# Performance work log

Measured on AMD Instinct MI355X. Metric: run time of the kernel, lower is better.

## Reference

```python
import jax, jax.numpy as jnp
import numpy as np

N = 150000
E = 600000
IN_DIM = 128
HID = 64


def setup_inputs() -> dict:
    key = jax.random.key(0)
    ks = jax.random.split(key, 8)
    obs = jax.random.normal(ks[0], (N, IN_DIM), dtype=jnp.float32)
    edge_index = jax.random.randint(ks[1], (2, E), 0, N, dtype=jnp.int64)
    # GCNConv / Linear parameters (PyTorch layout: W is [out, in])
    W1 = jax.random.normal(ks[2], (HID, IN_DIM), dtype=jnp.float32) / np.sqrt(IN_DIM)
    b1 = jnp.zeros((HID,), dtype=jnp.float32)
    W2 = jax.random.normal(ks[3], (HID, HID), dtype=jnp.float32) / np.sqrt(HID)
    b2 = jnp.zeros((HID,), dtype=jnp.float32)
    W3 = jax.random.normal(ks[4], (1, HID), dtype=jnp.float32) / np.sqrt(HID)
    b3 = jnp.zeros((1,), dtype=jnp.float32)
    return {"obs": obs, "edge_index": edge_index, "W1": W1, "b1": b1,
            "W2": W2, "b2": b2, "W3": W3, "b3": b3}


def _gcn_norm(edge_index, n):
    # PyG gcn_norm: add self-loops, symmetric normalization D^-1/2 A D^-1/2
    loops = jnp.arange(n, dtype=edge_index.dtype)
    row = jnp.concatenate([edge_index[0], loops])  # source
    col = jnp.concatenate([edge_index[1], loops])  # target
    deg = jax.ops.segment_sum(jnp.ones(row.shape[0], jnp.float32), col, num_segments=n)
    dinv = jnp.where(deg > 0, jax.lax.rsqrt(deg), 0.0)
    norm = dinv[row] * dinv[col]  # [E+N]
    return row, col, norm


def _gcn_conv(x, row, col, norm, n, W, b):
    # x' = lin(x); out[col] += norm * x'[row]; out += bias
    xw = x @ W.T                     # [N, out]
    msg = xw[row] * norm[:, None]    # gather + scale, [E+N, out]
    out = jax.ops.segment_sum(msg, col, num_segments=n)
    return out + b


def reference(obs, edge_index, W1, b1, W2, b2, W3, b3):
    n = obs.shape[0]
    row, col, norm = _gcn_norm(edge_index, n)
    h1 = jax.nn.relu(_gcn_conv(obs, row, col, norm, n, W1, b1))
    h2 = jax.nn.relu(_gcn_conv(h1, row, col, norm, n, W2, b2))
    out = h2 @ W3.T + b3             # [N, 1]
    out = out.reshape(-1, 15)[:, 3:].reshape(-1)  # drop first 3 of every 15
    return out
```

## Files before the change

kernel.cpp:

```cpp
#include <hip/hip_runtime.h>

#define NN 150000
#define NE 600000
#define IND 128
#define HID 64
#define KMAX 32
#define BSHIFT 8
#define NBUCK 586
#define SUBCAP 224
#define PARTB 293
#define GEMM_GRID ((NN + 63) / 64)
#define NOUT 120000

typedef short s16x8 __attribute__((ext_vector_type(8)));
typedef float f32x4 __attribute__((ext_vector_type(4)));

__device__ __forceinline__ unsigned f2bf(float f) {
    unsigned u = __float_as_uint(f);
    return (u + 0x7FFFu + ((u >> 16) & 1u)) >> 16;
}

#define ACC4(v, dr) \
    a0 = fmaf(__uint_as_float((v).x << 16), dr, a0); \
    a1 = fmaf(__uint_as_float((v).x & 0xFFFF0000u), dr, a1); \
    a2 = fmaf(__uint_as_float((v).y << 16), dr, a2); \
    a3 = fmaf(__uint_as_float((v).y & 0xFFFF0000u), dr, a3);

__global__ void k_zero(int* __restrict__ gcnt) {
    int t = blockIdx.x * 256 + threadIdx.x;
    if (t < NBUCK * 8) gcnt[t] = 0;
}

__global__ __launch_bounds__(256) void k_part(
        const int* __restrict__ rowv, const int* __restrict__ colv,
        int* __restrict__ gcnt, int2* __restrict__ ebuf) {
    __shared__ int hist[NBUCK];
    __shared__ int bases[NBUCK];
    int tid = threadIdx.x;
    for (int i = tid; i < NBUCK; i += 256) hist[i] = 0;
    __syncthreads();
    int4 r4[2], c4[2];
    int bk[8], sl[8];
    bool val[2];
    #pragma unroll
    for (int h = 0; h < 2; ++h) {
        int t = blockIdx.x * 512 + h * 256 + tid;
        val[h] = (t < NE / 4);
        if (val[h]) {
            r4[h] = ((const int4*)rowv)[t];
            c4[h] = ((const int4*)colv)[t];
            bk[4*h+0] = c4[h].x >> BSHIFT; sl[4*h+0] = atomicAdd(&hist[bk[4*h+0]], 1);
            bk[4*h+1] = c4[h].y >> BSHIFT; sl[4*h+1] = atomicAdd(&hist[bk[4*h+1]], 1);
            bk[4*h+2] = c4[h].z >> BSHIFT; sl[4*h+2] = atomicAdd(&hist[bk[4*h+2]], 1);
            bk[4*h+3] = c4[h].w >> BSHIFT; sl[4*h+3] = atomicAdd(&hist[bk[4*h+3]], 1);
        }
    }
    __syncthreads();
    int xcd = blockIdx.x & 7;
    for (int i = tid; i < NBUCK; i += 256)
        bases[i] = hist[i] ? atomicAdd(&gcnt[i * 8 + xcd], hist[i]) : 0;
    __syncthreads();
    #pragma unroll
    for (int h = 0; h < 2; ++h) {
        if (val[h]) {
            #pragma unroll
            for (int e = 0; e < 4; ++e) {
                int c = (e == 0) ? c4[h].x : (e == 1) ? c4[h].y : (e == 2) ? c4[h].z : c4[h].w;
                int r = (e == 0) ? r4[h].x : (e == 1) ? r4[h].y : (e == 2) ? r4[h].z : r4[h].w;
                int p = bases[bk[4*h+e]] + sl[4*h+e];
                if (p < SUBCAP) ebuf[(bk[4*h+e] * 8 + xcd) * SUBCAP + p] = make_int2(c, r);
            }
        }
    }
}

__global__ __launch_bounds__(256) void k_sort_gemm1(
        const float* __restrict__ obs, const float* __restrict__ W1,
        unsigned short* __restrict__ xs,
        const int* __restrict__ gcnt, const int2* __restrict__ ebuf,
        int* __restrict__ cursor, float* __restrict__ dinvf,
        int* __restrict__ csr_src) {
    __shared__ char smem[2 * 64 * IND * 2];
    int tid = threadIdx.x;
    if (blockIdx.x < NBUCK) {
        int k = blockIdx.x;
        int lo = k << BSHIFT;
        int* cnt = (int*)smem;
        cnt[tid] = 0;
        int lens[8];
        #pragma unroll
        for (int x = 0; x < 8; ++x) {
            int l = gcnt[k * 8 + x];
            lens[x] = l > SUBCAP ? SUBCAP : l;
        }
        __syncthreads();
        for (int x = 0; x < 8; ++x) {
            const int2* run = ebuf + (size_t)(k * 8 + x) * SUBCAP;
            for (int i = tid; i < lens[x]; i += 256) {
                int2 e = run[i];
                int s = atomicAdd(&cnt[e.x - lo], 1);
                if (s < KMAX) csr_src[e.x * KMAX + s] = e.y;
            }
        }
        __syncthreads();
        int n = lo + tid;
        if (n < NN) {
            cursor[n] = cnt[tid];
            dinvf[n] = rsqrtf((float)(cnt[tid] + 1));
        }
        return;
    }
    char* sA = smem;
    char* sW = smem + 64 * IND * 2;
    int base = (blockIdx.x - NBUCK) * 64;

    {
        const float4* Wsrc = (const float4*)W1;
        for (int idx = tid; idx < 64 * 32; idx += 256) {
            int row = idx >> 5, c4i = idx & 31;
            float4 w = Wsrc[idx];
            uint2 p;
            p.x = f2bf(w.x) | (f2bf(w.y) << 16);
            p.y = f2bf(w.z) | (f2bf(w.w) << 16);
            int byte = row * (IND * 2) + c4i * 8;
            byte ^= (row & 7) << 4;
            *(uint2*)(sW + byte) = p;
        }
    }
    {
        const float4* Xsrc = (const float4*)obs;
        for (int idx = tid; idx < 64 * 32; idx += 256) {
            int row = idx >> 5, c4i = idx & 31;
            int n = base + row; if (n >= NN) n = NN - 1;
            float4 v = Xsrc[(size_t)n * 32 + c4i];
            uint2 p;
            p.x = f2bf(v.x) | (f2bf(v.y) << 16);
            p.y = f2bf(v.z) | (f2bf(v.w) << 16);
            int byte = row * (IND * 2) + c4i * 8;
            byte ^= (row & 7) << 4;
            *(uint2*)(sA + byte) = p;
        }
    }
    __syncthreads();

    int wave = tid >> 6, lane = tid & 63;
    int wr = wave >> 1, wc = wave & 1;
    int r16 = lane & 15, kg = lane >> 4;

    f32x4 acc[2][2];
    #pragma unroll
    for (int i = 0; i < 2; ++i)
        #pragma unroll
        for (int j = 0; j < 2; ++j)
            acc[i][j] = (f32x4){0.f, 0.f, 0.f, 0.f};

    #pragma unroll
    for (int s = 0; s < IND / 32; ++s) {
        int kb = (s * 32 + kg * 8) * 2;
        s16x8 a[2], b[2];
        #pragma unroll
        for (int i = 0; i < 2; ++i) {
            int row = 32 * wr + 16 * i + r16;
            int byte = row * (IND * 2) + kb;
            byte ^= (row & 7) << 4;
            a[i] = *(const s16x8*)(sA + byte);
        }
        #pragma unroll
        for (int j = 0; j < 2; ++j) {
            int row = 32 * wc + 16 * j + r16;
            int byte = row * (IND * 2) + kb;
            byte ^= (row & 7) << 4;
            b[j] = *(const s16x8*)(sW + byte);
        }
        #pragma unroll
        for (int i = 0; i < 2; ++i)
            #pragma unroll
            for (int j = 0; j < 2; ++j)
                acc[i][j] = __builtin_amdgcn_mfma_f32_16x16x32_bf16(a[i], b[j], acc[i][j], 0, 0, 0);
    }

    __syncthreads();
    unsigned short* sC = (unsigned short*)sA;
    #pragma unroll
    for (int i = 0; i < 2; ++i) {
        #pragma unroll
        for (int r = 0; r < 4; ++r) {
            int nloc = 32 * wr + 16 * i + kg * 4 + r;
            #pragma unroll
            for (int j = 0; j < 2; ++j) {
                int c = 32 * wc + 16 * j + r16;
                sC[nloc * 64 + c] = (unsigned short)f2bf(acc[i][j][r]);
            }
        }
    }
    __syncthreads();
    {
        uint4* dst = (uint4*)(xs + (size_t)base * HID);
        const uint4* s4p = (const uint4*)sC;
        #pragma unroll
        for (int k2 = 0; k2 < 2; ++k2) {
            int idx = k2 * 256 + tid;
            if (base + (idx >> 3) < NN) dst[idx] = s4p[idx];
        }
    }
}

__global__ __launch_bounds__(256) void k_agg_gemm(
        const unsigned short* __restrict__ xs, const int* __restrict__ cursor,
        const float* __restrict__ dinvf, const int* __restrict__ csr_src,
        const float* __restrict__ bias, const float* __restrict__ W2,
        unsigned short* __restrict__ xs2) {
    __shared__ char smem[2 * 64 * HID * 2];
    char* sA = smem;
    char* sB = smem + 64 * HID * 2;
    int tid = threadIdx.x;
    int base = blockIdx.x * 64;

    {
        const float4* Wsrc = (const float4*)W2;
        for (int idx = tid; idx < 64 * 16; idx += 256) {
            int row = idx >> 4, c4i = idx & 15;
            float4 w = Wsrc[idx];
            uint2 p;
            p.x = f2bf(w.x) | (f2bf(w.y) << 16);
            p.y = f2bf(w.z) | (f2bf(w.w) << 16);
            int byte = row * (HID * 2) + c4i * 8;
            byte ^= (row & 7) << 4;
            *(uint2*)(sB + byte) = p;
        }
    }

    int lane = tid & 63;
    int l16 = lane & 15, gbase = lane & 48;
    int grp = tid >> 4;
    const uint2* src = (const uint2*)xs;
    float4 bb = ((const float4*)bias)[l16];

    int degA[4], cntA[4], idxA[4];
    uint2 svA[4];
    float drA[4];
    #pragma unroll
    for (int s4 = 0; s4 < 4; ++s4) {
        int node = base + s4 * 16 + grp;
        bool ok = node < NN;
        int nc = ok ? node : NN - 1;
        int deg = cursor[nc];
        degA[s4] = deg;
        cntA[s4] = ok ? (deg < KMAX ? deg : KMAX) : 0;
        idxA[s4] = csr_src[nc * KMAX + l16];
        svA[s4]  = src[(size_t)nc * 16 + l16];
    }
    #pragma unroll
    for (int s4 = 0; s4 < 4; ++s4) {
        drA[s4] = (l16 < cntA[s4]) ? dinvf[idxA[s4]] : 0.0f;
    }

    #pragma unroll
    for (int s4 = 0; s4 < 4; ++s4) {
        int row = s4 * 16 + grp;
        int node = base + row;
        int cnt = cntA[s4];
        float dn = rsqrtf((float)(degA[s4] + 1));
        uint2 sv = svA[s4];
        float a0 = __uint_as_float(sv.x << 16) * dn;
        float a1 = __uint_as_float(sv.x & 0xFFFF0000u) * dn;
        float a2 = __uint_as_float(sv.y << 16) * dn;
        float a3 = __uint_as_float(sv.y & 0xFFFF0000u) * dn;
        uint2 v[8];
        #pragma unroll
        for (int j = 0; j < 8; ++j) {
            int r = __shfl(idxA[s4], gbase + j, 64);
            r = (j < cnt) ? r : 0;
            v[j] = src[(size_t)r * 16 + l16];
        }
        #pragma unroll
        for (int j = 0; j < 8; ++j) {
            float dr = __shfl(drA[s4], gbase + j, 64);
            ACC4(v[j], dr)
        }
        if (cnt > 8) {
            int c16 = cnt < 16 ? cnt : 16;
            for (int j = 8; j < c16; ++j) {
                int r    = __shfl(idxA[s4], gbase + j, 64);
                float dr = __shfl(drA[s4], gbase + j, 64);
                uint2 vv = src[(size_t)r * 16 + l16];
                ACC4(vv, dr)
            }
            for (int j = 16; j < cnt; ++j) {
                int r = csr_src[node * KMAX + j];
                float dr = dinvf[r];
                uint2 vv = src[(size_t)r * 16 + l16];
                ACC4(vv, dr)
            }
        }
        float h0 = fmaxf(fmaf(dn, a0, bb.x), 0.f);
        float h1 = fmaxf(fmaf(dn, a1, bb.y), 0.f);
        float h2 = fmaxf(fmaf(dn, a2, bb.z), 0.f);
        float h3 = fmaxf(fmaf(dn, a3, bb.w), 0.f);
        uint2 o;
        o.x = f2bf(h0) | (f2bf(h1) << 16);
        o.y = f2bf(h2) | (f2bf(h3) << 16);
        if (node >= NN) { o.x = 0u; o.y = 0u; }
        int byte = row * (HID * 2) + l16 * 8;
        byte ^= (row & 7) << 4;
        *(uint2*)(sA + byte) = o;
    }
    __syncthreads();

    int wave = tid >> 6;
    int wr = wave >> 1, wc = wave & 1;
    int r16 = lane & 15, kg = lane >> 4;

    f32x4 acc[2][2];
    #pragma unroll
    for (int i = 0; i < 2; ++i)
        #pragma unroll
        for (int j = 0; j < 2; ++j)
            acc[i][j] = (f32x4){0.f, 0.f, 0.f, 0.f};

    #pragma unroll
    for (int s = 0; s < HID / 32; ++s) {
        int kb = (s * 32 + kg * 8) * 2;
        s16x8 a[2], bfr[2];
        #pragma unroll
        for (int i = 0; i < 2; ++i) {
            int row = 32 * wr + 16 * i + r16;
            int byte = row * (HID * 2) + kb;
            byte ^= (row & 7) << 4;
            a[i] = *(const s16x8*)(sA + byte);
        }
        #pragma unroll
        for (int j = 0; j < 2; ++j) {
            int row = 32 * wc + 16 * j + r16;
            int byte = row * (HID * 2) + kb;
            byte ^= (row & 7) << 4;
            bfr[j] = *(const s16x8*)(sB + byte);
        }
        #pragma unroll
        for (int i = 0; i < 2; ++i)
            #pragma unroll
            for (int j = 0; j < 2; ++j)
                acc[i][j] = __builtin_amdgcn_mfma_f32_16x16x32_bf16(a[i], bfr[j], acc[i][j], 0, 0, 0);
    }

    __syncthreads();
    unsigned short* sC = (unsigned short*)sA;
    #pragma unroll
    for (int i = 0; i < 2; ++i) {
        #pragma unroll
        for (int r = 0; r < 4; ++r) {
            int nloc = 32 * wr + 16 * i + kg * 4 + r;
            int n = base + nloc;
            float d = dinvf[n < NN ? n : NN - 1];
            #pragma unroll
            for (int j = 0; j < 2; ++j) {
                int c = 32 * wc + 16 * j + r16;
                sC[nloc * 64 + c] = (unsigned short)f2bf(acc[i][j][r] * d);
            }
        }
    }
    __syncthreads();
    {
        uint4* dst = (uint4*)(xs2 + (size_t)base * HID);
        const uint4* s4p = (const uint4*)sC;
        #pragma unroll
        for (int k2 = 0; k2 < 2; ++k2) {
            int idx = k2 * 256 + tid;
            if (base + (idx >> 3) < NN) dst[idx] = s4p[idx];
        }
    }
}

__global__ __launch_bounds__(256) void k_agg_out(const unsigned short* __restrict__ xs,
                      const int* __restrict__ cursor, const int* __restrict__ csr_src,
                      const float* __restrict__ bias, const float* __restrict__ W3,
                      const float* __restrict__ b3, float* __restrict__ outp) {
    int tid = threadIdx.x;
    int lane = tid & 63;
    int l16 = lane & 15, gbase = lane & 48;
    int q = blockIdx.x * 16 + (tid >> 4);
    if (q >= NOUT) return;
    int g15 = q / 12, jj12 = q - g15 * 12;
    int node = g15 * 15 + 3 + jj12;
    int deg = cursor[node];
    int cnt = deg < KMAX ? deg : KMAX;
    float dn = rsqrtf((float)(deg + 1));
    const uint2* src = (const uint2*)xs;
    int idx0 = csr_src[node * KMAX + l16];
    float w0 = (l16 < cnt) ? 1.0f : 0.0f;
    uint2 sv = src[(size_t)node * 16 + l16];
    float a0 = __uint_as_float(sv.x << 16);
    float a1 = __uint_as_float(sv.x & 0xFFFF0000u);
    float a2 = __uint_as_float(sv.y << 16);
    float a3 = __uint_as_float(sv.y & 0xFFFF0000u);
    uint2 v[8];
    #pragma unroll
    for (int j = 0; j < 8; ++j) {
        int r = __shfl(idx0, gbase + j, 64);
        r = (j < cnt) ? r : 0;
        v[j] = src[(size_t)r * 16 + l16];
    }
    #pragma unroll
    for (int j = 0; j < 8; ++j) {
        float w = __shfl(w0, gbase + j, 64);
        ACC4(v[j], w)
    }
    if (cnt > 8) {
        int c16 = cnt < 16 ? cnt : 16;
        for (int j = 8; j < c16; ++j) {
            int r = __shfl(idx0, gbase + j, 64);
            uint2 vv = src[(size_t)r * 16 + l16];
            ACC4(vv, 1.0f)
        }
        for (int j = 16; j < cnt; ++j) {
            int r = csr_src[node * KMAX + j];
            uint2 vv = src[(size_t)r * 16 + l16];
            ACC4(vv, 1.0f)
        }
    }
    float4 bb = ((const float4*)bias)[l16];
    float h0 = fmaxf(fmaf(dn, a0, bb.x), 0.f);
    float h1 = fmaxf(fmaf(dn, a1, bb.y), 0.f);
    float h2 = fmaxf(fmaf(dn, a2, bb.z), 0.f);
    float h3 = fmaxf(fmaf(dn, a3, bb.w), 0.f);
    float4 ww = ((const float4*)W3)[l16];
    float v3 = h0 * ww.x + h1 * ww.y + h2 * ww.z + h3 * ww.w;
    v3 += __shfl_xor(v3, 1, 64);
    v3 += __shfl_xor(v3, 2, 64);
    v3 += __shfl_xor(v3, 4, 64);
    v3 += __shfl_xor(v3, 8, 64);
    if (l16 == 0) outp[q] = v3 + b3[0];
}

extern "C" void kernel_launch(void* const* d_in, const int* in_sizes, int n_in,
                              void* d_out, int out_size, void* d_ws, size_t ws_size,
                              hipStream_t stream) {
    const float* obs = (const float*)d_in[0];
    const int*   ei  = (const int*)d_in[1];
    const float* W1  = (const float*)d_in[2];
    const float* b1  = (const float*)d_in[3];
    const float* W2  = (const float*)d_in[4];
    const float* b2  = (const float*)d_in[5];
    const float* W3  = (const float*)d_in[6];
    const float* b3  = (const float*)d_in[7];
    float* out = (float*)d_out;

    char* ws = (char*)d_ws;
    size_t off = 0;
    auto alloc = [&](size_t bytes) -> void* {
        void* p = ws + off;
        off += (bytes + 255) & ~(size_t)255;
        return p;
    };
    int*   gcnt    = (int*)  alloc((size_t)NBUCK * 8 * 4);
    int*   cursor  = (int*)  alloc((size_t)NN * 4);
    float* dinvf   = (float*)alloc((size_t)NN * 4);
    int*   csr_src = (int*)  alloc((size_t)NN * KMAX * 4);
    int2*  ebuf    = (int2*) alloc((size_t)NBUCK * 8 * SUBCAP * 8);
    unsigned short* XB  = (unsigned short*)alloc((size_t)NN * HID * 2);
    unsigned short* XB2 = (unsigned short*)alloc((size_t)NN * HID * 2);

    const int* rowv = ei;
    const int* colv = ei + NE;

    k_zero<<<(NBUCK * 8 + 255) / 256, 256, 0, stream>>>(gcnt);
    k_part<<<PARTB, 256, 0, stream>>>(rowv, colv, gcnt, ebuf);
    k_sort_gemm1<<<NBUCK + GEMM_GRID, 256, 0, stream>>>(obs, W1, XB, gcnt, ebuf,
                                                        cursor, dinvf, csr_src);
    k_agg_gemm<<<GEMM_GRID, 256, 0, stream>>>(XB, cursor, dinvf, csr_src, b1, W2, XB2);
    k_agg_out<<<(NOUT + 15) / 16, 256, 0, stream>>>(XB2, cursor, csr_src, b2, W3, b3, out);
}
```

Baseline: 93.36 us.

## Load obs fp32 tiles directly into LDS and precompute swizzled bf16 W1

The first GEMM stage now stages raw fp32 obs rows straight into shared memory with global_load_lds, using a swizzled source address, and converts them to bf16 at fragment-read time with v_cvt_pk_bf16_f32. The bf16 conversion and swizzle of W1 move into the initial zeroing kernel, and each GEMM block copies the prepared 16KB buffer via direct-to-LDS loads. This removes the per-block register round trip and conversion for both operands. In exchange the kernel's LDS use grows from 32KB to 48KB, which can lower occupancy, and the conversion now happens in the MFMA loop.

```diff
diff --git a/kernel.cpp b/kernel.cpp
--- a/kernel.cpp
+++ b/kernel.cpp
@@ -20,15 +20,35 @@
     return (u + 0x7FFFu + ((u >> 16) & 1u)) >> 16;
 }
 
+__device__ __forceinline__ unsigned cvtpk(float lo, float hi) {
+    unsigned r;
+    asm("v_cvt_pk_bf16_f32 %0, %1, %2" : "=v"(r) : "v"(lo), "v"(hi));
+    return r;
+}
+
 #define ACC4(v, dr) \
     a0 = fmaf(__uint_as_float((v).x << 16), dr, a0); \
     a1 = fmaf(__uint_as_float((v).x & 0xFFFF0000u), dr, a1); \
     a2 = fmaf(__uint_as_float((v).y << 16), dr, a2); \
     a3 = fmaf(__uint_as_float((v).y & 0xFFFF0000u), dr, a3);
 
-__global__ void k_zero(int* __restrict__ gcnt) {
+__global__ void k_pre(int* __restrict__ gcnt, const float* __restrict__ W1,
+                      unsigned char* __restrict__ W1s) {
     int t = blockIdx.x * 256 + threadIdx.x;
     if (t < NBUCK * 8) gcnt[t] = 0;
+    if (t < 1024) {
+        int row = t >> 4, g = t & 15;
+        const float4* w4 = (const float4*)W1;
+        float4 lo = w4[row * 32 + g * 2];
+        float4 hi = w4[row * 32 + g * 2 + 1];
+        uint4 p;
+        p.x = f2bf(lo.x) | (f2bf(lo.y) << 16);
+        p.y = f2bf(lo.z) | (f2bf(lo.w) << 16);
+        p.z = f2bf(hi.x) | (f2bf(hi.y) << 16);
+        p.w = f2bf(hi.z) | (f2bf(hi.w) << 16);
+        int byte = row * 256 + ((g * 16) ^ ((row & 7) << 4));
+        *(uint4*)(W1s + byte) = p;
+    }
 }
 
 __global__ __launch_bounds__(256) void k_part(
@@ -75,12 +95,12 @@
 }
 
 __global__ __launch_bounds__(256) void k_sort_gemm1(
-        const float* __restrict__ obs, const float* __restrict__ W1,
+        const float* __restrict__ obs, const unsigned char* __restrict__ W1s,
         unsigned short* __restrict__ xs,
         const int* __restrict__ gcnt, const int2* __restrict__ ebuf,
         int* __restrict__ cursor, float* __restrict__ dinvf,
         int* __restrict__ csr_src) {
-    __shared__ char smem[2 * 64 * IND * 2];
+    __shared__ char smem[48 * 1024];
     int tid = threadIdx.x;
     if (blockIdx.x < NBUCK) {
         int k = blockIdx.x;
@@ -111,39 +131,30 @@
         return;
     }
     char* sA = smem;
-    char* sW = smem + 64 * IND * 2;
+    char* sW = smem + 32 * 1024;
     int base = (blockIdx.x - NBUCK) * 64;
 
-    {
-        const float4* Wsrc = (const float4*)W1;
-        for (int idx = tid; idx < 64 * 32; idx += 256) {
-            int row = idx >> 5, c4i = idx & 31;
-            float4 w = Wsrc[idx];
-            uint2 p;
-            p.x = f2bf(w.x) | (f2bf(w.y) << 16);
-            p.y = f2bf(w.z) | (f2bf(w.w) << 16);
-            int byte = row * (IND * 2) + c4i * 8;
-            byte ^= (row & 7) << 4;
-            *(uint2*)(sW + byte) = p;
-        }
-    }
-    {
-        const float4* Xsrc = (const float4*)obs;
-        for (int idx = tid; idx < 64 * 32; idx += 256) {
-            int row = idx >> 5, c4i = idx & 31;
-            int n = base + row; if (n >= NN) n = NN - 1;
-            float4 v = Xsrc[(size_t)n * 32 + c4i];
-            uint2 p;
-            p.x = f2bf(v.x) | (f2bf(v.y) << 16);
-            p.y = f2bf(v.z) | (f2bf(v.w) << 16);
-            int byte = row * (IND * 2) + c4i * 8;
-            byte ^= (row & 7) << 4;
-            *(uint2*)(sA + byte) = p;
-        }
-    }
-    __syncthreads();
-
     int wave = tid >> 6, lane = tid & 63;
+
+    #pragma unroll
+    for (int i = 0; i < 4; ++i) {
+        int c = wave * 4 + i;
+        __builtin_amdgcn_global_load_lds(
+            (const unsigned int*)(W1s + c * 1024 + lane * 16),
+            (unsigned int*)(sW + c * 1024), 16, 0, 0);
+    }
+    #pragma unroll
+    for (int i = 0; i < 8; ++i) {
+        int c = wave * 8 + i;
+        int rowl = 2 * c + (lane >> 5);
+        int n = base + rowl; if (n >= NN) n = NN - 1;
+        int gsrc = (lane & 31) ^ (rowl & 7);
+        __builtin_amdgcn_global_load_lds(
+            (const unsigned int*)((const char*)obs + (size_t)n * 512 + gsrc * 16),
+            (unsigned int*)(sA + c * 1024), 16, 0, 0);
+    }
+    __syncthreads();
+
     int wr = wave >> 1, wc = wave & 1;
     int r16 = lane & 15, kg = lane >> 4;
 
@@ -156,15 +167,22 @@
 
     #pragma unroll
     for (int s = 0; s < IND / 32; ++s) {
-        int kb = (s * 32 + kg * 8) * 2;
         s16x8 a[2], b[2];
         #pragma unroll
         for (int i = 0; i < 2; ++i) {
             int row = 32 * wr + 16 * i + r16;
-            int byte = row * (IND * 2) + kb;
-            byte ^= (row & 7) << 4;
-            a[i] = *(const s16x8*)(sA + byte);
-        }
+            int g = s * 8 + kg * 2;
+            int sw = row & 7;
+            float4 lo4 = *(const float4*)(sA + row * 512 + ((g ^ sw) << 4));
+            float4 hi4 = *(const float4*)(sA + row * 512 + (((g + 1) ^ sw) << 4));
+            uint4 av;
+            av.x = cvtpk(lo4.x, lo4.y);
+            av.y = cvtpk(lo4.z, lo4.w);
+            av.z = cvtpk(hi4.x, hi4.y);
+            av.w = cvtpk(hi4.z, hi4.w);
+            a[i] = __builtin_bit_cast(s16x8, av);
+        }
+        int kb = (s * 32 + kg * 8) * 2;
         #pragma unroll
         for (int j = 0; j < 2; ++j) {
             int row = 32 * wc + 16 * j + r16;
@@ -457,15 +475,16 @@
     float* dinvf   = (float*)alloc((size_t)NN * 4);
     int*   csr_src = (int*)  alloc((size_t)NN * KMAX * 4);
     int2*  ebuf    = (int2*) alloc((size_t)NBUCK * 8 * SUBCAP * 8);
+    unsigned char* W1s = (unsigned char*)alloc(16 * 1024);
     unsigned short* XB  = (unsigned short*)alloc((size_t)NN * HID * 2);
     unsigned short* XB2 = (unsigned short*)alloc((size_t)NN * HID * 2);
 
     const int* rowv = ei;
     const int* colv = ei + NE;
 
-    k_zero<<<(NBUCK * 8 + 255) / 256, 256, 0, stream>>>(gcnt);
+    k_pre <<<(NBUCK * 8 + 255) / 256, 256, 0, stream>>>(gcnt, W1, W1s);
     k_part<<<PARTB, 256, 0, stream>>>(rowv, colv, gcnt, ebuf);
-    k_sort_gemm1<<<NBUCK + GEMM_GRID, 256, 0, stream>>>(obs, W1, XB, gcnt, ebuf,
+    k_sort_gemm1<<<NBUCK + GEMM_GRID, 256, 0, stream>>>(obs, W1s, XB, gcnt, ebuf,
                                                         cursor, dinvf, csr_src);
     k_agg_gemm<<<GEMM_GRID, 256, 0, stream>>>(XB, cursor, dinvf, csr_src, b1, W2, XB2);
     k_agg_out<<<(NOUT + 15) / 16, 256, 0, stream>>>(XB2, cursor, csr_src, b2, W3, b3, out);
```

New measurement: 89.22 us. 4.4% less time.
